# Performance work log

Measured on AMD Instinct MI355X. Metric: run time of the kernel, lower is better.

## Reference

```python
import jax, jax.numpy as jnp
import numpy as np


def setup_inputs() -> dict:
    key = jax.random.key(0)
    k1, k2, k3 = jax.random.split(key, 3)
    B, C, H, W = 16, 256, 48, 48
    INTER = C // 2
    x = jax.random.normal(k1, (B, C, H, W), dtype=jnp.float32)
    # nn.init.normal_(weight, std=0.01); 1x1 conv kernels stored as (out, in)
    theta_w = 0.01 * jax.random.normal(k2, (INTER, C), dtype=jnp.float32)
    phi_w = 0.01 * jax.random.normal(k3, (INTER, C), dtype=jnp.float32)
    theta_b = jnp.zeros((INTER,), dtype=jnp.float32)
    phi_b = jnp.zeros((INTER,), dtype=jnp.float32)
    return {"x": x, "theta_w": theta_w, "theta_b": theta_b, "phi_w": phi_w, "phi_b": phi_b}


def reference(x, theta_w, theta_b, phi_w, phi_b):
    b, c, h, w = x.shape
    inter = theta_w.shape[0]
    n = h * w
    # 1x1 conv == channel-wise linear projection
    theta_x = jnp.einsum('bchw,kc->bkhw', x, theta_w) + theta_b[None, :, None, None]
    phi_x = jnp.einsum('bchw,kc->bkhw', x, phi_w) + phi_b[None, :, None, None]
    q = theta_x.reshape(b, inter, n)   # [b, k, n]
    kmat = phi_x.reshape(b, inter, n)  # [b, k, n]
    g = x.reshape(b, c, n)             # [b, c, n]
    # f = theta^T @ phi : [b, n, n], scaled then softmaxed over last dim
    f = jnp.einsum('bkn,bkm->bnm', q, kmat) / jnp.sqrt(jnp.asarray(inter, x.dtype))
    f = jax.nn.softmax(f, axis=-1)
    # y = f @ g^T : [b, c, n]
    y = jnp.einsum('bnm,bcm->bcn', f, g)
    return y.reshape(b, c, h, w)
```

## Files before the change

kernel.cpp:

```cpp
#include <hip/hip_runtime.h>
#include <hip/hip_bf16.h>

#define B_SZ 16
#define C_IN 256
#define N_SP 2304
#define K_INT 128
#define NTILE 36
#define MT 32
#define MITER 72

typedef __attribute__((ext_vector_type(8))) short short8;
typedef __attribute__((ext_vector_type(4))) float f32x4;

__device__ __align__(16) short g_Wbf[2 * K_INT * C_IN];

__device__ inline unsigned pk_bf16(float a, float b) {
  float2 f; f.x = a; f.y = b;
  __hip_bfloat162 h = __float22bfloat162_rn(f);
  unsigned u;
  __builtin_memcpy(&u, &h, sizeof(u));
  return u;
}

__global__ __launch_bounds__(256) void wcvt_kernel(
    const float* __restrict__ tw, const float* __restrict__ pw)
{
  const int i = (blockIdx.x * 256 + threadIdx.x) * 4;
  float4 a = *(const float4*)(tw + i);
  float4 p = *(const float4*)(pw + i);
  uint2 ua; ua.x = pk_bf16(a.x, a.y); ua.y = pk_bf16(a.z, a.w);
  uint2 up; up.x = pk_bf16(p.x, p.y); up.y = pk_bf16(p.z, p.w);
  *(uint2*)(g_Wbf + i) = ua;
  *(uint2*)(g_Wbf + 32768 + i) = up;
}

__global__ __launch_bounds__(256) void proj_kernel(
    const float* __restrict__ x,
    const float* __restrict__ theta_b, const float* __restrict__ phi_b,
    short* __restrict__ Qt, short* __restrict__ Kt, short* __restrict__ Gbf)
{
  __shared__ short Xl[64][264];

  const int b  = blockIdx.x / NTILE;
  const int n0 = (blockIdx.x % NTILE) * 64;
  const int t  = threadIdx.x;

  {
    const float* xrow = x + ((size_t)b * C_IN + t) * N_SP + n0;
    unsigned tp[32];
#pragma unroll
    for (int i = 0; i < 16; ++i) {
      float4 v = ((const float4*)xrow)[i];
      tp[2*i]   = pk_bf16(v.x, v.y);
      tp[2*i+1] = pk_bf16(v.z, v.w);
    }
    uint4* grow = (uint4*)(Gbf + ((size_t)b * C_IN + t) * N_SP + n0);
#pragma unroll
    for (int i = 0; i < 8; ++i) {
      uint4 u; u.x = tp[4*i]; u.y = tp[4*i+1]; u.z = tp[4*i+2]; u.w = tp[4*i+3];
      grow[i] = u;
    }
#pragma unroll
    for (int j = 0; j < 32; ++j) {
      Xl[2*j][t]   = (short)tp[j];
      Xl[2*j+1][t] = (short)(tp[j] >> 16);
    }
  }
  __syncthreads();

  const int wave = t >> 6, lane = t & 63;
  const int col = lane & 15, quad = lane >> 4;

  f32x4 acc[2][2][4];
#pragma unroll
  for (int p = 0; p < 2; ++p)
#pragma unroll
    for (int kr = 0; kr < 2; ++kr)
#pragma unroll
      for (int j = 0; j < 4; ++j) {
        acc[p][kr][j][0] = 0.f; acc[p][kr][j][1] = 0.f;
        acc[p][kr][j][2] = 0.f; acc[p][kr][j][3] = 0.f;
      }

#pragma unroll
  for (int cs = 0; cs < 8; ++cs) {
    const int c0 = cs * 32;
    short8 afr[2][2];
#pragma unroll
    for (int p = 0; p < 2; ++p)
#pragma unroll
      for (int kr = 0; kr < 2; ++kr) {
        const int k = wave * 32 + kr * 16 + col;
        afr[p][kr] = *(const short8*)(g_Wbf + p * 32768 + k * C_IN + c0 + quad * 8);
      }
#pragma unroll
    for (int j = 0; j < 4; ++j) {
      short8 bfr = *(const short8*)&Xl[j * 16 + col][c0 + quad * 8];
#pragma unroll
      for (int p = 0; p < 2; ++p)
#pragma unroll
        for (int kr = 0; kr < 2; ++kr)
          acc[p][kr][j] = __builtin_amdgcn_mfma_f32_16x16x32_bf16(
              afr[p][kr], bfr, acc[p][kr][j], 0, 0, 0);
    }
  }

#pragma unroll
  for (int p = 0; p < 2; ++p) {
    const float* bias = p ? phi_b : theta_b;
    short* dst = p ? Kt : Qt;
#pragma unroll
    for (int kr = 0; kr < 2; ++kr) {
      const int k0 = wave * 32 + kr * 16 + quad * 4;
      float4 bv = *(const float4*)(bias + k0);
#pragma unroll
      for (int j = 0; j < 4; ++j) {
        const int n = n0 + j * 16 + col;
        f32x4 v = acc[p][kr][j];
        uint2 sv;
        sv.x = pk_bf16(v[0] + bv.x, v[1] + bv.y);
        sv.y = pk_bf16(v[2] + bv.z, v[3] + bv.w);
        *(uint2*)(dst + ((size_t)b * N_SP + n) * K_INT + k0) = sv;
      }
    }
  }
}

__global__ __launch_bounds__(256) void attn_kernel(
    const short* __restrict__ Qt, const short* __restrict__ Kt,
    const short* __restrict__ Gbf, float* __restrict__ out)
{
  __shared__ __align__(16) char smem[53504];
  float* l_lds = (float*)(smem + 53248);

  const int b   = blockIdx.x / NTILE;
  const int qn0 = (blockIdx.x % NTILE) * 64;
  const int t = threadIdx.x;
  const int wave = t >> 6, lane = t & 63;
  const int col = lane & 15, quad = lane >> 4;

  const short* Ktb = Kt  + (size_t)b * N_SP * K_INT;
  const short* Gb  = Gbf + (size_t)b * C_IN * N_SP;

  short8 qf[4];
  {
    const short* qb = Qt + ((size_t)b * N_SP + qn0 + wave * 16 + col) * K_INT + quad * 8;
#pragma unroll
    for (int kk = 0; kk < 4; ++kk) qf[kk] = *(const short8*)(qb + kk * 32);
  }

  f32x4 yacc[4][4];
#pragma unroll
  for (int i = 0; i < 4; ++i)
#pragma unroll
    for (int j = 0; j < 4; ++j) {
      yacc[i][j][0] = 0.f; yacc[i][j][1] = 0.f;
      yacc[i][j][2] = 0.f; yacc[i][j][3] = 0.f;
    }
  f32x4 lacc;
  lacc[0] = 0.f; lacc[1] = 0.f; lacc[2] = 0.f; lacc[3] = 0.f;

  short8 ones;
#pragma unroll
  for (int j = 0; j < 8; ++j) ones[j] = (short)0x3F80;

  const float SC2 = 0.12754859f;

  const int KW = (t >> 4) * 256 + (((t & 15) ^ ((((t >> 5) & 7)) << 1)) << 4);
  const int GW = 8192 + (t >> 2) * 64 + ((((t & 3) ^ ((t >> 3) & 3))) << 4);
  int KR[4];
#pragma unroll
  for (int kk = 0; kk < 4; ++kk)
    KR[kk] = col * 256 + ((((kk << 2) + quad) ^ ((((col >> 1) & 7)) << 1)) << 4);
  const int GR = 8192 + wave * 4096 + col * 64 + ((quad ^ ((col >> 1) & 3)) << 4);
  const int PW = 49152 + wave * 1024 + col * 64 + quad * 16;
  const int PR = 49152 + col * 64 + quad * 16;

  const int koff = (t >> 4) * K_INT + (t & 15) * 8;
  const int goff = (t >> 2) * N_SP + (t & 3) * 8;

  short8 pre[6];
  pre[0] = *(const short8*)(Ktb + koff);
  pre[1] = *(const short8*)(Ktb + 2048 + koff);
#pragma unroll
  for (int i = 0; i < 4; ++i) pre[2 + i] = *(const short8*)(Gb + i * 64 * N_SP + goff);
  *(short8*)(smem + KW) = pre[0];
  *(short8*)(smem + KW + 4096) = pre[1];
#pragma unroll
  for (int i = 0; i < 4; ++i) *(short8*)(smem + GW + i * 4096) = pre[2 + i];
  pre[0] = *(const short8*)(Ktb + 4096 + koff);
  pre[1] = *(const short8*)(Ktb + 6144 + koff);
#pragma unroll
  for (int i = 0; i < 4; ++i) pre[2 + i] = *(const short8*)(Gb + 32 + i * 64 * N_SP + goff);
  const short* kptr = Ktb + 8192 + koff;
  const short* gptr = Gb + 64 + goff;
  __syncthreads();

#define SUBITER(MTV, RD, WR)                                                   \
  {                                                                            \
    if ((MTV) + 1 < MITER) {                                                   \
      *(short8*)(smem + KW + (WR)) = pre[0];                                   \
      *(short8*)(smem + KW + (WR) + 4096) = pre[1];                            \
      _Pragma("unroll")                                                        \
      for (int i = 0; i < 4; ++i)                                              \
        *(short8*)(smem + GW + (WR) + i * 4096) = pre[2 + i];                  \
      if ((MTV) + 2 < MITER) {                                                 \
        pre[0] = *(const short8*)(kptr);                                       \
        pre[1] = *(const short8*)(kptr + 2048);                                \
        _Pragma("unroll")                                                      \
        for (int i = 0; i < 4; ++i)                                            \
          pre[2 + i] = *(const short8*)(gptr + i * 64 * N_SP);                 \
        kptr += 4096; gptr += 32;                                              \
      }                                                                        \
    }                                                                          \
    f32x4 s0, s1;                                                              \
    s0[0] = 0.f; s0[1] = 0.f; s0[2] = 0.f; s0[3] = 0.f;                        \
    s1[0] = 0.f; s1[1] = 0.f; s1[2] = 0.f; s1[3] = 0.f;                        \
    _Pragma("unroll")                                                          \
    for (int kk = 0; kk < 4; ++kk) {                                           \
      short8 a0 = *(const short8*)(smem + KR[kk] + (RD));                      \
      s0 = __builtin_amdgcn_mfma_f32_16x16x32_bf16(a0, qf[kk], s0, 0, 0, 0);   \
      short8 a1 = *(const short8*)(smem + KR[kk] + (RD) + 4096);               \
      s1 = __builtin_amdgcn_mfma_f32_16x16x32_bf16(a1, qf[kk], s1, 0, 0, 0);   \
    }                                                                          \
    unsigned u0 = pk_bf16(exp2f(s0[0] * SC2), exp2f(s0[1] * SC2));             \
    unsigned u1 = pk_bf16(exp2f(s0[2] * SC2), exp2f(s0[3] * SC2));             \
    unsigned u2 = pk_bf16(exp2f(s1[0] * SC2), exp2f(s1[1] * SC2));             \
    unsigned u3 = pk_bf16(exp2f(s1[2] * SC2), exp2f(s1[3] * SC2));             \
    asm("v_permlane32_swap_b32 %0, %1" : "+v"(u0), "+v"(u2));                  \
    asm("v_permlane32_swap_b32 %0, %1" : "+v"(u1), "+v"(u3));                  \
    asm("v_permlane16_swap_b32 %0, %1" : "+v"(u0), "+v"(u2));                  \
    asm("v_permlane16_swap_b32 %0, %1" : "+v"(u1), "+v"(u3));                  \
    unsigned uu[4] = {u0, u1, u2, u3};                                         \
    short8 pa; __builtin_memcpy(&pa, uu, 16);                                  \
    lacc = __builtin_amdgcn_mfma_f32_16x16x32_bf16(pa, ones, lacc, 0, 0, 0);   \
    *(short8*)(smem + PW) = pa;                                                \
    __syncthreads();                               \
    short8 paq[4];                                                             \
    _Pragma("unroll")                                                          \
    for (int qt = 0; qt < 4; ++qt)                                             \
      paq[qt] = *(const short8*)(smem + PR + qt * 1024);                       \
    _Pragma("unroll")                                                          \
    for (int ct = 0; ct < 4; ++ct) {                                           \
      short8 gb = *(const short8*)(smem + GR + (RD) + ct * 1024);              \
      _Pragma("unroll")                                                        \
      for (int qt = 0; qt < 4; ++qt)                                           \
        yacc[qt][ct] = __builtin_amdgcn_mfma_f32_16x16x32_bf16(                \
            paq[qt], gb, yacc[qt][ct], 0, 0, 0);                               \
    }                                                                          \
    __syncthreads();          \
  }

  for (int mt2 = 0; mt2 < MITER / 2; ++mt2) {
    SUBITER(2 * mt2, 0, 24576)
    SUBITER(2 * mt2 + 1, 24576, 0)
  }
#undef SUBITER

  if (col == 0) {
#pragma unroll
    for (int r = 0; r < 4; ++r) l_lds[wave * 16 + quad * 4 + r] = lacc[r];
  }
  __syncthreads();

#pragma unroll
  for (int qt = 0; qt < 4; ++qt) {
    float4 lq = *(const float4*)&l_lds[qt * 16 + quad * 4];
    float4 iv;
    iv.x = 1.0f / lq.x; iv.y = 1.0f / lq.y; iv.z = 1.0f / lq.z; iv.w = 1.0f / lq.w;
    const int nb = qn0 + qt * 16 + quad * 4;
#pragma unroll
    for (int ct = 0; ct < 4; ++ct) {
      const int c = wave * 64 + ct * 16 + col;
      f32x4 v = yacc[qt][ct];
      float4 o;
      o.x = v[0] * iv.x; o.y = v[1] * iv.y; o.z = v[2] * iv.z; o.w = v[3] * iv.w;
      *(float4*)(out + ((size_t)b * C_IN + c) * N_SP + nb) = o;
    }
  }
}

extern "C" void kernel_launch(void* const* d_in, const int* in_sizes, int n_in,
                              void* d_out, int out_size, void* d_ws, size_t ws_size,
                              hipStream_t stream) {
  const float* x  = (const float*)d_in[0];
  const float* tw = (const float*)d_in[1];
  const float* tb = (const float*)d_in[2];
  const float* pw = (const float*)d_in[3];
  const float* pb = (const float*)d_in[4];
  float* out = (float*)d_out;

  short* Qt  = (short*)d_ws;
  short* Kt  = Qt + (size_t)B_SZ * N_SP * K_INT;
  short* Gbf = Kt + (size_t)B_SZ * N_SP * K_INT;

  wcvt_kernel<<<32, 256, 0, stream>>>(tw, pw);
  proj_kernel<<<B_SZ * NTILE, 256, 0, stream>>>(x, tb, pb, Qt, Kt, Gbf);
  attn_kernel<<<B_SZ * NTILE, 256, 0, stream>>>(Qt, Kt, Gbf, out);
}
```

Before: 257.3 us.

## Load K and G fragments directly from global, drop LDS staging

Removes the LDS staging and double-buffered prefetch of K and G tiles. Each wave now loads its MFMA operand fragments straight from global memory into registers. P is exchanged through a small double-buffered LDS array, which drops one of the two barriers per iteration. This cuts LDS traffic, barrier count and shared-memory footprint, which may raise occupancy. The cost is that every wave loads K redundantly, global loads are less coalesced, and load latency is less hidden because each fetch is only one iteration ahead.

```diff
diff --git a/kernel.cpp b/kernel.cpp
--- a/kernel.cpp
+++ b/kernel.cpp
@@ -130,8 +130,8 @@
     const short* __restrict__ Qt, const short* __restrict__ Kt,
     const short* __restrict__ Gbf, float* __restrict__ out)
 {
-  __shared__ __align__(16) char smem[53504];
-  float* l_lds = (float*)(smem + 53248);
+  __shared__ __align__(16) short Pblob[2][4][64][8];
+  __shared__ float l_lds[64];
 
   const int b   = blockIdx.x / NTILE;
   const int qn0 = (blockIdx.x % NTILE) * 64;
@@ -166,96 +166,65 @@
 
   const float SC2 = 0.12754859f;
 
-  const int KW = (t >> 4) * 256 + (((t & 15) ^ ((((t >> 5) & 7)) << 1)) << 4);
-  const int GW = 8192 + (t >> 2) * 64 + ((((t & 3) ^ ((t >> 3) & 3))) << 4);
-  int KR[4];
-#pragma unroll
-  for (int kk = 0; kk < 4; ++kk)
-    KR[kk] = col * 256 + ((((kk << 2) + quad) ^ ((((col >> 1) & 7)) << 1)) << 4);
-  const int GR = 8192 + wave * 4096 + col * 64 + ((quad ^ ((col >> 1) & 3)) << 4);
-  const int PW = 49152 + wave * 1024 + col * 64 + quad * 16;
-  const int PR = 49152 + col * 64 + quad * 16;
-
-  const int koff = (t >> 4) * K_INT + (t & 15) * 8;
-  const int goff = (t >> 2) * N_SP + (t & 3) * 8;
-
-  short8 pre[6];
-  pre[0] = *(const short8*)(Ktb + koff);
-  pre[1] = *(const short8*)(Ktb + 2048 + koff);
-#pragma unroll
-  for (int i = 0; i < 4; ++i) pre[2 + i] = *(const short8*)(Gb + i * 64 * N_SP + goff);
-  *(short8*)(smem + KW) = pre[0];
-  *(short8*)(smem + KW + 4096) = pre[1];
-#pragma unroll
-  for (int i = 0; i < 4; ++i) *(short8*)(smem + GW + i * 4096) = pre[2 + i];
-  pre[0] = *(const short8*)(Ktb + 4096 + koff);
-  pre[1] = *(const short8*)(Ktb + 6144 + koff);
-#pragma unroll
-  for (int i = 0; i < 4; ++i) pre[2 + i] = *(const short8*)(Gb + 32 + i * 64 * N_SP + goff);
-  const short* kptr = Ktb + 8192 + koff;
-  const short* gptr = Gb + 64 + goff;
-  __syncthreads();
-
-#define SUBITER(MTV, RD, WR)                                                   \
-  {                                                                            \
-    if ((MTV) + 1 < MITER) {                                                   \
-      *(short8*)(smem + KW + (WR)) = pre[0];                                   \
-      *(short8*)(smem + KW + (WR) + 4096) = pre[1];                            \
-      _Pragma("unroll")                                                        \
-      for (int i = 0; i < 4; ++i)                                              \
-        *(short8*)(smem + GW + (WR) + i * 4096) = pre[2 + i];                  \
-      if ((MTV) + 2 < MITER) {                                                 \
-        pre[0] = *(const short8*)(kptr);                                       \
-        pre[1] = *(const short8*)(kptr + 2048);                                \
-        _Pragma("unroll")                                                      \
-        for (int i = 0; i < 4; ++i)                                            \
-          pre[2 + i] = *(const short8*)(gptr + i * 64 * N_SP);                 \
-        kptr += 4096; gptr += 32;                                              \
-      }                                                                        \
-    }                                                                          \
-    f32x4 s0, s1;                                                              \
-    s0[0] = 0.f; s0[1] = 0.f; s0[2] = 0.f; s0[3] = 0.f;                        \
-    s1[0] = 0.f; s1[1] = 0.f; s1[2] = 0.f; s1[3] = 0.f;                        \
-    _Pragma("unroll")                                                          \
-    for (int kk = 0; kk < 4; ++kk) {                                           \
-      short8 a0 = *(const short8*)(smem + KR[kk] + (RD));                      \
-      s0 = __builtin_amdgcn_mfma_f32_16x16x32_bf16(a0, qf[kk], s0, 0, 0, 0);   \
-      short8 a1 = *(const short8*)(smem + KR[kk] + (RD) + 4096);               \
-      s1 = __builtin_amdgcn_mfma_f32_16x16x32_bf16(a1, qf[kk], s1, 0, 0, 0);   \
-    }                                                                          \
-    unsigned u0 = pk_bf16(exp2f(s0[0] * SC2), exp2f(s0[1] * SC2));             \
-    unsigned u1 = pk_bf16(exp2f(s0[2] * SC2), exp2f(s0[3] * SC2));             \
-    unsigned u2 = pk_bf16(exp2f(s1[0] * SC2), exp2f(s1[1] * SC2));             \
-    unsigned u3 = pk_bf16(exp2f(s1[2] * SC2), exp2f(s1[3] * SC2));             \
-    asm("v_permlane32_swap_b32 %0, %1" : "+v"(u0), "+v"(u2));                  \
-    asm("v_permlane32_swap_b32 %0, %1" : "+v"(u1), "+v"(u3));                  \
-    asm("v_permlane16_swap_b32 %0, %1" : "+v"(u0), "+v"(u2));                  \
-    asm("v_permlane16_swap_b32 %0, %1" : "+v"(u1), "+v"(u3));                  \
-    unsigned uu[4] = {u0, u1, u2, u3};                                         \
-    short8 pa; __builtin_memcpy(&pa, uu, 16);                                  \
-    lacc = __builtin_amdgcn_mfma_f32_16x16x32_bf16(pa, ones, lacc, 0, 0, 0);   \
-    *(short8*)(smem + PW) = pa;                                                \
-    __syncthreads();                               \
-    short8 paq[4];                                                             \
-    _Pragma("unroll")                                                          \
-    for (int qt = 0; qt < 4; ++qt)                                             \
-      paq[qt] = *(const short8*)(smem + PR + qt * 1024);                       \
-    _Pragma("unroll")                                                          \
-    for (int ct = 0; ct < 4; ++ct) {                                           \
-      short8 gb = *(const short8*)(smem + GR + (RD) + ct * 1024);              \
-      _Pragma("unroll")                                                        \
-      for (int qt = 0; qt < 4; ++qt)                                           \
-        yacc[qt][ct] = __builtin_amdgcn_mfma_f32_16x16x32_bf16(                \
-            paq[qt], gb, yacc[qt][ct], 0, 0, 0);                               \
-    }                                                                          \
-    __syncthreads();          \
-  }
-
-  for (int mt2 = 0; mt2 < MITER / 2; ++mt2) {
-    SUBITER(2 * mt2, 0, 24576)
-    SUBITER(2 * mt2 + 1, 24576, 0)
-  }
-#undef SUBITER
+  const short* kptr = Ktb + col * K_INT + quad * 8;
+  const short* gptr = Gb + ((size_t)(wave * 64 + col)) * N_SP + quad * 8;
+
+  short8 kf[8];
+#pragma unroll
+  for (int kk = 0; kk < 4; ++kk) {
+    kf[2 * kk]     = *(const short8*)(kptr + kk * 32);
+    kf[2 * kk + 1] = *(const short8*)(kptr + 2048 + kk * 32);
+  }
+
+  for (int mt = 0; mt < MITER; ++mt) {
+    f32x4 s0, s1;
+    s0[0] = 0.f; s0[1] = 0.f; s0[2] = 0.f; s0[3] = 0.f;
+    s1[0] = 0.f; s1[1] = 0.f; s1[2] = 0.f; s1[3] = 0.f;
+#pragma unroll
+    for (int kk = 0; kk < 4; ++kk) {
+      s0 = __builtin_amdgcn_mfma_f32_16x16x32_bf16(kf[2 * kk],     qf[kk], s0, 0, 0, 0);
+      s1 = __builtin_amdgcn_mfma_f32_16x16x32_bf16(kf[2 * kk + 1], qf[kk], s1, 0, 0, 0);
+    }
+
+    short8 gb[4];
+#pragma unroll
+    for (int ct = 0; ct < 4; ++ct)
+      gb[ct] = *(const short8*)(gptr + (size_t)ct * 16 * N_SP + mt * 32);
+
+    unsigned u0 = pk_bf16(exp2f(s0[0] * SC2), exp2f(s0[1] * SC2));
+    unsigned u1 = pk_bf16(exp2f(s0[2] * SC2), exp2f(s0[3] * SC2));
+    unsigned u2 = pk_bf16(exp2f(s1[0] * SC2), exp2f(s1[1] * SC2));
+    unsigned u3 = pk_bf16(exp2f(s1[2] * SC2), exp2f(s1[3] * SC2));
+    asm("v_permlane32_swap_b32 %0, %1" : "+v"(u0), "+v"(u2));
+    asm("v_permlane32_swap_b32 %0, %1" : "+v"(u1), "+v"(u3));
+    asm("v_permlane16_swap_b32 %0, %1" : "+v"(u0), "+v"(u2));
+    asm("v_permlane16_swap_b32 %0, %1" : "+v"(u1), "+v"(u3));
+    unsigned uu[4] = {u0, u1, u2, u3};
+    short8 pa; __builtin_memcpy(&pa, uu, 16);
+
+    lacc = __builtin_amdgcn_mfma_f32_16x16x32_bf16(pa, ones, lacc, 0, 0, 0);
+
+    *(short8*)&Pblob[mt & 1][wave][lane][0] = pa;
+    __syncthreads();
+
+    if (mt + 1 < MITER) {
+      const short* kp = kptr + (size_t)(mt + 1) * 4096;
+#pragma unroll
+      for (int kk = 0; kk < 4; ++kk) {
+        kf[2 * kk]     = *(const short8*)(kp + kk * 32);
+        kf[2 * kk + 1] = *(const short8*)(kp + 2048 + kk * 32);
+      }
+    }
+
+#pragma unroll
+    for (int qt = 0; qt < 4; ++qt) {
+      short8 paq = *(const short8*)&Pblob[mt & 1][qt][lane][0];
+#pragma unroll
+      for (int ct = 0; ct < 4; ++ct)
+        yacc[qt][ct] = __builtin_amdgcn_mfma_f32_16x16x32_bf16(
+            paq, gb[ct], yacc[qt][ct], 0, 0, 0);
+    }
+  }
 
   if (col == 0) {
 #pragma unroll
```

Result: slower. 405.2 us (+57.5%).

## Load G operand directly into registers and drop one barrier per iteration

Applied to the files above, without the earlier changes.

The G (value) tiles are no longer staged through shared memory. Each wave now loads its own G fragments from global memory straight into registers, double-buffered across iterations. The P tile and K tile buffers are double-buffered so that only one __syncthreads per sub-iteration is needed instead of two, and the K swizzle pattern changes. The aim is to cut LDS traffic and barrier stalls, at the cost of global loads that are less coalesced (16-byte strided rows) and more register pressure.

```diff
diff --git a/kernel.cpp b/kernel.cpp
--- a/kernel.cpp
+++ b/kernel.cpp
@@ -130,8 +130,9 @@
     const short* __restrict__ Qt, const short* __restrict__ Kt,
     const short* __restrict__ Gbf, float* __restrict__ out)
 {
-  __shared__ __align__(16) char smem[53504];
-  float* l_lds = (float*)(smem + 53248);
+  __shared__ __align__(16) char Kl[2][8192];
+  __shared__ __align__(16) short Pblob[2][4][64][8];
+  __shared__ float l_lds[64];
 
   const int b   = blockIdx.x / NTILE;
   const int qn0 = (blockIdx.x % NTILE) * 64;
@@ -166,63 +167,42 @@
 
   const float SC2 = 0.12754859f;
 
-  const int KW = (t >> 4) * 256 + (((t & 15) ^ ((((t >> 5) & 7)) << 1)) << 4);
-  const int GW = 8192 + (t >> 2) * 64 + ((((t & 3) ^ ((t >> 3) & 3))) << 4);
-  int KR[4];
+  const int KW0 = (t >> 4) * 256 + ((((t & 15) ^ ((t >> 4) & 7))) << 4);
+  int KR0[4];
 #pragma unroll
   for (int kk = 0; kk < 4; ++kk)
-    KR[kk] = col * 256 + ((((kk << 2) + quad) ^ ((((col >> 1) & 7)) << 1)) << 4);
-  const int GR = 8192 + wave * 4096 + col * 64 + ((quad ^ ((col >> 1) & 3)) << 4);
-  const int PW = 49152 + wave * 1024 + col * 64 + quad * 16;
-  const int PR = 49152 + col * 64 + quad * 16;
+    KR0[kk] = col * 256 + ((((kk << 2) + quad) ^ (col & 7)) << 4);
 
   const int koff = (t >> 4) * K_INT + (t & 15) * 8;
-  const int goff = (t >> 2) * N_SP + (t & 3) * 8;
-
-  short8 pre[6];
-  pre[0] = *(const short8*)(Ktb + koff);
-  pre[1] = *(const short8*)(Ktb + 2048 + koff);
-#pragma unroll
-  for (int i = 0; i < 4; ++i) pre[2 + i] = *(const short8*)(Gb + i * 64 * N_SP + goff);
-  *(short8*)(smem + KW) = pre[0];
-  *(short8*)(smem + KW + 4096) = pre[1];
-#pragma unroll
-  for (int i = 0; i < 4; ++i) *(short8*)(smem + GW + i * 4096) = pre[2 + i];
-  pre[0] = *(const short8*)(Ktb + 4096 + koff);
-  pre[1] = *(const short8*)(Ktb + 6144 + koff);
-#pragma unroll
-  for (int i = 0; i < 4; ++i) pre[2 + i] = *(const short8*)(Gb + 32 + i * 64 * N_SP + goff);
-  const short* kptr = Ktb + 8192 + koff;
-  const short* gptr = Gb + 64 + goff;
+  const short* gbase = Gb + ((size_t)(wave * 64 + col)) * N_SP + quad * 8;
+
+  short8 krA, krB;
+  krA = *(const short8*)(Ktb + koff);
+  krB = *(const short8*)(Ktb + 2048 + koff);
+  *(short8*)(Kl[0] + KW0) = krA;
+  *(short8*)(Kl[0] + KW0 + 4096) = krB;
+  krA = *(const short8*)(Ktb + 4096 + koff);
+  krB = *(const short8*)(Ktb + 6144 + koff);
+  short8 gA[4], gB[4];
+#pragma unroll
+  for (int ct = 0; ct < 4; ++ct)
+    gA[ct] = *(const short8*)(gbase + (size_t)ct * 16 * N_SP);
   __syncthreads();
 
-#define SUBITER(MTV, RD, WR)                                                   \
+#define SUBITER(MTV, CUR, GC, GN)                                              \
   {                                                                            \
-    if ((MTV) + 1 < MITER) {                                                   \
-      *(short8*)(smem + KW + (WR)) = pre[0];                                   \
-      *(short8*)(smem + KW + (WR) + 4096) = pre[1];                            \
-      _Pragma("unroll")                                                        \
-      for (int i = 0; i < 4; ++i)                                              \
-        *(short8*)(smem + GW + (WR) + i * 4096) = pre[2 + i];                  \
-      if ((MTV) + 2 < MITER) {                                                 \
-        pre[0] = *(const short8*)(kptr);                                       \
-        pre[1] = *(const short8*)(kptr + 2048);                                \
-        _Pragma("unroll")                                                      \
-        for (int i = 0; i < 4; ++i)                                            \
-          pre[2 + i] = *(const short8*)(gptr + i * 64 * N_SP);                 \
-        kptr += 4096; gptr += 32;                                              \
-      }                                                                        \
-    }                                                                          \
+                           \
     f32x4 s0, s1;                                                              \
     s0[0] = 0.f; s0[1] = 0.f; s0[2] = 0.f; s0[3] = 0.f;                        \
     s1[0] = 0.f; s1[1] = 0.f; s1[2] = 0.f; s1[3] = 0.f;                        \
     _Pragma("unroll")                                                          \
     for (int kk = 0; kk < 4; ++kk) {                                           \
-      short8 a0 = *(const short8*)(smem + KR[kk] + (RD));                      \
+      short8 a0 = *(const short8*)(Kl[CUR] + KR0[kk]);                         \
       s0 = __builtin_amdgcn_mfma_f32_16x16x32_bf16(a0, qf[kk], s0, 0, 0, 0);   \
-      short8 a1 = *(const short8*)(smem + KR[kk] + (RD) + 4096);               \
+      short8 a1 = *(const short8*)(Kl[CUR] + KR0[kk] + 4096);                  \
       s1 = __builtin_amdgcn_mfma_f32_16x16x32_bf16(a1, qf[kk], s1, 0, 0, 0);   \
     }                                                                          \
+                    \
     unsigned u0 = pk_bf16(exp2f(s0[0] * SC2), exp2f(s0[1] * SC2));             \
     unsigned u1 = pk_bf16(exp2f(s0[2] * SC2), exp2f(s0[3] * SC2));             \
     unsigned u2 = pk_bf16(exp2f(s1[0] * SC2), exp2f(s1[1] * SC2));             \
@@ -234,26 +214,41 @@
     unsigned uu[4] = {u0, u1, u2, u3};                                         \
     short8 pa; __builtin_memcpy(&pa, uu, 16);                                  \
     lacc = __builtin_amdgcn_mfma_f32_16x16x32_bf16(pa, ones, lacc, 0, 0, 0);   \
-    *(short8*)(smem + PW) = pa;                                                \
-    __syncthreads();                               \
-    short8 paq[4];                                                             \
+                         \
+    *(short8*)&Pblob[CUR][wave][lane][0] = pa;                                 \
+           \
+    if ((MTV) + 1 < MITER) {                                                   \
+      *(short8*)(Kl[(CUR) ^ 1] + KW0) = krA;                                   \
+      *(short8*)(Kl[(CUR) ^ 1] + KW0 + 4096) = krB;                            \
+    }                                                                          \
+                      \
+    if ((MTV) + 2 < MITER) {                                                   \
+      const short* kp = Ktb + (size_t)((MTV) + 2) * 4096 + koff;               \
+      krA = *(const short8*)(kp);                                              \
+      krB = *(const short8*)(kp + 2048);                                       \
+    }                                                                          \
+               \
+    if ((MTV) + 1 < MITER) {                                                   \
+      _Pragma("unroll")                                                        \
+      for (int ct = 0; ct < 4; ++ct)                                           \
+        GN[ct] = *(const short8*)(gbase + (size_t)ct * 16 * N_SP +             \
+                                  ((MTV) + 1) * 32);                           \
+    }                                                                          \
+    __syncthreads();                                                           \
+        \
     _Pragma("unroll")                                                          \
-    for (int qt = 0; qt < 4; ++qt)                                             \
-      paq[qt] = *(const short8*)(smem + PR + qt * 1024);                       \
-    _Pragma("unroll")                                                          \
-    for (int ct = 0; ct < 4; ++ct) {                                           \
-      short8 gb = *(const short8*)(smem + GR + (RD) + ct * 1024);              \
+    for (int qt = 0; qt < 4; ++qt) {                                           \
+      short8 paq = *(const short8*)&Pblob[CUR][qt][lane][0];                   \
       _Pragma("unroll")                                                        \
-      for (int qt = 0; qt < 4; ++qt)                                           \
+      for (int ct = 0; ct < 4; ++ct)                                           \
         yacc[qt][ct] = __builtin_amdgcn_mfma_f32_16x16x32_bf16(                \
-            paq[qt], gb, yacc[qt][ct], 0, 0, 0);                               \
-    }                                                                          \
-    __syncthreads();          \
+            paq, GC[ct], yacc[qt][ct], 0, 0, 0);                               \
+    }                                                                          \
   }
 
   for (int mt2 = 0; mt2 < MITER / 2; ++mt2) {
-    SUBITER(2 * mt2, 0, 24576)
-    SUBITER(2 * mt2 + 1, 24576, 0)
+    SUBITER(2 * mt2,     0, gA, gB)
+    SUBITER(2 * mt2 + 1, 1, gB, gA)
   }
 #undef SUBITER
 
```

New measurement: 245.3 us. 1.05x faster.
